# Kernel optimization log

Hardware: AMD Instinct MI355X
Metric: run time of the kernel (lower is better)

## Reference

```python
import jax, jax.numpy as jnp
import numpy as np

D_MODEL = 1024
N_HEAD = 16
HEAD_DIM = D_MODEL // N_HEAD
D_INNER = (int(D_MODEL * 2.0) + 7) // 8 * 8  # 2048
EPS = 1e-6


def setup_inputs() -> dict:
    key = jax.random.key(0)
    ks = jax.random.split(key, 8)
    B, T = 2, 2048
    s = 0.02
    return {
        "x": jax.random.normal(ks[0], (B, T, D_MODEL), dtype=jnp.float32),
        "ln1_w": jnp.ones((D_MODEL,), jnp.float32),
        "ln2_w": jnp.ones((D_MODEL,), jnp.float32),
        "qkv_w": jax.random.normal(ks[1], (3 * D_MODEL, D_MODEL), jnp.float32) * s,
        "o_w": jax.random.normal(ks[2], (D_MODEL, D_MODEL), jnp.float32) * s,
        "gate_w": jax.random.normal(ks[3], (D_INNER, D_MODEL), jnp.float32) * s,
        "up_w": jax.random.normal(ks[4], (D_INNER, D_MODEL), jnp.float32) * s,
        "down_w": jax.random.normal(ks[5], (D_MODEL, D_INNER), jnp.float32) * s,
    }


def _rmsnorm(x, w):
    xf = x.astype(jnp.float32)
    rms = jax.lax.rsqrt(jnp.mean(xf * xf, axis=-1, keepdims=True) + EPS)
    return (xf * rms).astype(x.dtype) * w


def _attention(x, qkv_w, o_w):
    B, T, D = x.shape
    qkv = (x @ qkv_w.T).reshape(B, T, 3, N_HEAD, HEAD_DIM)
    q, k, v = qkv[:, :, 0], qkv[:, :, 1], qkv[:, :, 2]  # [B,T,H,hd]
    scale = 1.0 / np.sqrt(HEAD_DIM)
    att = jnp.einsum("bqhd,bkhd->bhqk", q, k) * scale
    causal = jnp.tril(jnp.ones((T, T), dtype=bool))
    att = jnp.where(causal[None, None], att, -jnp.inf)
    att = jax.nn.softmax(att, axis=-1)
    y = jnp.einsum("bhqk,bkhd->bqhd", att, v).reshape(B, T, D)
    return y @ o_w.T


def _ffn(x, gate_w, up_w, down_w):
    g = jax.nn.silu(x @ gate_w.T)
    u = x @ up_w.T
    return (g * u) @ down_w.T


def reference(x, ln1_w, ln2_w, qkv_w, o_w, gate_w, up_w, down_w):
    x = x + _attention(_rmsnorm(x, ln1_w), qkv_w, o_w)
    x = x + _ffn(_rmsnorm(x, ln2_w), gate_w, up_w, down_w)
    return x
```

## Files before the change

### kernel.cpp

```cpp
#include <hip/hip_runtime.h>
#include <hip/hip_bf16.h>
#include <cstdint>

typedef __hip_bfloat16 bf16;
typedef __attribute__((ext_vector_type(8))) short bf16x8;
typedef __attribute__((ext_vector_type(4))) float f32x4;
typedef __attribute__((ext_vector_type(4))) int i32x4;

#define T_SEQ 2048
#define DMODEL 1024
#define NHEAD 16
#define DHEAD 64
#define MROWS 4096

typedef const __attribute__((address_space(1))) void* gas_ptr;
typedef __attribute__((address_space(3))) void* las_ptr;

static __device__ __forceinline__ f32x4 mfma16(bf16x8 a, bf16x8 b, f32x4 c) {
  return __builtin_amdgcn_mfma_f32_16x16x32_bf16(a, b, c, 0, 0, 0);
}
static __device__ __forceinline__ void gload_lds16(const void* g, void* l) {
  __builtin_amdgcn_global_load_lds((gas_ptr)g, (las_ptr)l, 16, 0, 0);
}
static __device__ __forceinline__ float b2f(unsigned short u) {
  union { unsigned int i; float f; } x; x.i = ((unsigned int)u) << 16; return x.f;
}
static __device__ __forceinline__ unsigned short f2bu(float f) {
  __hip_bfloat16 h = __float2bfloat16(f);
  unsigned short u; __builtin_memcpy(&u, &h, 2); return u;
}
static __device__ __forceinline__ int tpack(float a, float b) {
  const unsigned ua = __builtin_bit_cast(unsigned, a);
  const unsigned ub = __builtin_bit_cast(unsigned, b);
  return (int)((ua >> 16) | (ub & 0xFFFF0000u));
}

__global__ __launch_bounds__(256) void prep_k(const float* __restrict__ a,
                                              const float* __restrict__ b,
                                              const float* __restrict__ c,
                                              const float* __restrict__ d,
                                              const float* __restrict__ e,
                                              bf16* __restrict__ out,
                                              const float* __restrict__ x,
                                              const float* __restrict__ ln1w,
                                              bf16* __restrict__ H) {
  if (blockIdx.x < 10240) {
    const int idx = (blockIdx.x * 256 + threadIdx.x) * 4;
    const float* src;
    int off, dst;
    if (idx < 3145728) {
      src = a; off = idx; dst = idx;
    } else if (idx < 4194304) {
      src = b; off = idx - 3145728; dst = idx;
    } else if (idx < 6291456) {
      src = c; off = idx - 4194304;
      dst = 4194304 + ((off >> 10) << 11) + (off & 1023);
    } else if (idx < 8388608) {
      src = d; off = idx - 6291456;
      dst = 4194304 + ((off >> 10) << 11) + 1024 + (off & 1023);
    } else {
      src = e; off = idx - 8388608; dst = idx;
    }
    const float4 v = *(const float4*)(src + off);
    ushort4 ov;
    ov.x = f2bu(v.x); ov.y = f2bu(v.y); ov.z = f2bu(v.z); ov.w = f2bu(v.w);
    *(ushort4*)((unsigned short*)out + dst) = ov;
  } else {
    const int row = blockIdx.x - 10240;
    const int tid = threadIdx.x;
    const float4 v = ((const float4*)(x + (size_t)row * DMODEL))[tid];
    float ss = v.x * v.x + v.y * v.y + v.z * v.z + v.w * v.w;
#pragma unroll
    for (int off = 32; off; off >>= 1) ss += __shfl_xor(ss, off);
    __shared__ float red[4];
    if ((tid & 63) == 0) red[tid >> 6] = ss;
    __syncthreads();
    const float tot = red[0] + red[1] + red[2] + red[3];
    const float rinv = rsqrtf(tot * (1.f / DMODEL) + 1e-6f);
    const float4 wv = ((const float4*)ln1w)[tid];
    bf16* o = H + (size_t)row * DMODEL + tid * 4;
    o[0] = __float2bfloat16(v.x * rinv * wv.x);
    o[1] = __float2bfloat16(v.y * rinv * wv.y);
    o[2] = __float2bfloat16(v.z * rinv * wv.z);
    o[3] = __float2bfloat16(v.w * rinv * wv.w);
  }
}

__global__ __launch_bounds__(256) void rms_k(const float* __restrict__ x,
                                             const float* __restrict__ w,
                                             bf16* __restrict__ out) {
  const int row = blockIdx.x;
  const int tid = threadIdx.x;
  const float4 v = ((const float4*)(x + (size_t)row * DMODEL))[tid];
  float ss = v.x * v.x + v.y * v.y + v.z * v.z + v.w * v.w;
#pragma unroll
  for (int off = 32; off; off >>= 1) ss += __shfl_xor(ss, off);
  __shared__ float red[4];
  if ((tid & 63) == 0) red[tid >> 6] = ss;
  __syncthreads();
  const float tot = red[0] + red[1] + red[2] + red[3];
  const float rinv = rsqrtf(tot * (1.f / DMODEL) + 1e-6f);
  const float4 wv = ((const float4*)w)[tid];
  bf16* o = out + (size_t)row * DMODEL + tid * 4;
  o[0] = __float2bfloat16(v.x * rinv * wv.x);
  o[1] = __float2bfloat16(v.y * rinv * wv.y);
  o[2] = __float2bfloat16(v.z * rinv * wv.z);
  o[3] = __float2bfloat16(v.w * rinv * wv.w);
}

template <int K, int EPI>
__global__ __launch_bounds__(256) void gemm_bt(const bf16* __restrict__ A,
                                               const bf16* __restrict__ Bw, int N,
                                               void* __restrict__ o0, void* __restrict__ o1,
                                               void* __restrict__ o2,
                                               const float* __restrict__ res) {
  __shared__ bf16 As[128 * 64];
  __shared__ bf16 Bs[128 * 64];
  const int bn0 = blockIdx.x * 128;
  const int bm0 = blockIdx.y * 128;
  const int tid = threadIdx.x;
  const int wave = tid >> 6, lane = tid & 63;
  const int wr = wave >> 1, wc = wave & 1;
  const int fr = lane & 15, u = lane >> 4, r4 = u * 4;
  const int srow = lane >> 3;
  const int sslot = (lane & 7) ^ srow;
  const int fsw = fr & 7;

  const f32x4 fzero = {0.f, 0.f, 0.f, 0.f};
  f32x4 acc[4][4];
#pragma unroll
  for (int i = 0; i < 4; i++)
#pragma unroll
    for (int j = 0; j < 4; j++) acc[i][j] = fzero;

  const bf16* gA = A + (size_t)(bm0 + wave * 32 + srow) * K + sslot * 8;
  const bf16* gB = Bw + (size_t)(bn0 + wave * 32 + srow) * K + sslot * 8;

  for (int k0 = 0; k0 < K; k0 += 64) {
#pragma unroll
    for (int j = 0; j < 4; j++)
      gload_lds16(gA + (size_t)(j * 8) * K + k0, &As[(wave * 32 + j * 8) * 64]);
#pragma unroll
    for (int j = 0; j < 4; j++)
      gload_lds16(gB + (size_t)(j * 8) * K + k0, &Bs[(wave * 32 + j * 8) * 64]);
    __syncthreads();
#pragma unroll
    for (int kh = 0; kh < 2; kh++) {
      const int slot8 = ((kh * 4 + u) ^ fsw) * 8;
      bf16x8 af[4], bfr[4];
#pragma unroll
      for (int mr = 0; mr < 4; mr++)
        af[mr] = *(const bf16x8*)&As[(wr * 64 + mr * 16 + fr) * 64 + slot8];
#pragma unroll
      for (int nr = 0; nr < 4; nr++)
        bfr[nr] = *(const bf16x8*)&Bs[(wc * 64 + nr * 16 + fr) * 64 + slot8];
#pragma unroll
      for (int mr = 0; mr < 4; mr++)
#pragma unroll
        for (int nr = 0; nr < 4; nr++)
          acc[mr][nr] = mfma16(af[mr], bfr[nr], acc[mr][nr]);
    }
    __syncthreads();
  }

#pragma unroll
  for (int mr = 0; mr < 4; mr++) {
#pragma unroll
    for (int nr = 0; nr < 4; nr++) {
      if (EPI == 1) {
        const int col = bn0 + wc * 64 + nr * 16 + fr;
        const int sel = col >> 10;
        const int n = col & 1023;
        const int h = n >> 6, d = n & 63;
        const int row0 = bm0 + wr * 64 + mr * 16 + r4;
        const int b = row0 >> 11, t0 = row0 & 2047;
        if (sel == 2) {
          ushort4 ov;
          ov.x = f2bu(acc[mr][nr][0]);
          ov.y = f2bu(acc[mr][nr][1]);
          ov.z = f2bu(acc[mr][nr][2]);
          ov.w = f2bu(acc[mr][nr][3]);
          *(ushort4*)((unsigned short*)o2 +
                      (((size_t)(b * NHEAD + h)) * DHEAD + d) * T_SEQ + t0) = ov;
        } else {
          bf16* dst = (sel == 0) ? (bf16*)o0 : (bf16*)o1;
#pragma unroll
          for (int r = 0; r < 4; r++)
            dst[(((size_t)(b * NHEAD + h)) * T_SEQ + t0 + r) * DHEAD + d] =
                __float2bfloat16(acc[mr][nr][r]);
        }
      } else {
#pragma unroll
        for (int r = 0; r < 4; r++) {
          const int row = bm0 + wr * 64 + mr * 16 + r4 + r;
          const int col = bn0 + wc * 64 + nr * 16 + fr;
          const float vsum = acc[mr][nr][r];
          if (EPI == 2) {
            ((float*)o0)[(size_t)row * N + col] = res[(size_t)row * N + col] + vsum;
          } else {
            const float other = __shfl_xor(vsum, 1);
            if ((fr & 1) == 0) {
              const float g = vsum, uu = other;
              const float s = g / (1.f + __expf(-g));
              ((bf16*)o0)[(size_t)row * (N >> 1) + (col >> 1)] =
                  __float2bfloat16(s * uu);
            }
          }
        }
      }
    }
  }
}

__global__ __launch_bounds__(256) void attn_k(const bf16* __restrict__ qb,
                                              const bf16* __restrict__ kb,
                                              const bf16* __restrict__ vt,
                                              bf16* __restrict__ y,
                                              unsigned short* __restrict__ pO,
                                              float* __restrict__ pL) {
  const int wave = threadIdx.x >> 6, lane = threadIdx.x & 63;
  const int bid = blockIdx.x;
  int bh, qt, ks0, nb, heavy, hs;
  if (bid < 1024) {
    const int c = bid & 7, r = bid >> 3;
    bh = c * 4 + (r & 3);
    const int idx = r >> 2;
    qt = 31 - (idx >> 1);
    hs = idx & 1;
    heavy = 1;
    nb = qt + 1;
    ks0 = hs * nb;
  } else {
    const int bd = bid - 1024;
    const int c = bd & 7, r = bd >> 3;
    bh = c * 4 + (r & 3);
    qt = 15 - (r >> 2);
    hs = 0;
    heavy = 0;
    nb = 2 * qt + 2;
    ks0 = 0;
  }
  const int b = bh >> 4, h = bh & 15;
  const int fr = lane & 15, g8 = (lane >> 4) * 8, r4 = (lane >> 4) * 4;
  const int u = lane >> 4;
  const int src1 = fr + ((u & 1) << 5);
  const int src2 = src1 + 16;
  const bool hB = u >= 2;

  const bf16* qp = qb + (size_t)bh * T_SEQ * DHEAD;
  const bf16* kp = kb + (size_t)bh * T_SEQ * DHEAD;
  const bf16* vp = vt + (size_t)bh * DHEAD * T_SEQ;

  __shared__ char Ks[2][4096];
  __shared__ char Vs[2][4096];

  const int q0 = qt * 64 + wave * 16;
  const int kend = q0 + 16;
  const int qrow = q0 + fr;

  const bf16x8 qf0 = *(const bf16x8*)(qp + (size_t)(q0 + fr) * DHEAD + g8);
  const bf16x8 qf1 = *(const bf16x8*)(qp + (size_t)(q0 + fr) * DHEAD + 32 + g8);

  const int krow_l = lane >> 3;
  const int kslot_l = (lane & 7) ^ krow_l;
  const int vrow_l = lane >> 2;
  const int vslot_l = (lane & 3) ^ ((lane >> 3) & 3);

  const int kswz = (fr & 7) << 4;
  const int koffA = fr * 128 + ((u * 16) ^ kswz);
  const int koffB = fr * 128 + (((4 + u) * 16) ^ kswz);
  const int vswz = ((fr >> 1) & 3) << 4;

  const f32x4 fzero = {0.f, 0.f, 0.f, 0.f};
  f32x4 acc[4];
  float lpart = 0.f;
#pragma unroll
  for (int nf = 0; nf < 4; nf++) acc[nf] = fzero;

  gload_lds16(kp + (size_t)(ks0 * 32 + wave * 8 + krow_l) * DHEAD + kslot_l * 8,
              &Ks[0][wave * 1024]);
  gload_lds16(vp + (size_t)(wave * 16 + vrow_l) * T_SEQ + ks0 * 32 + vslot_l * 8,
              &Vs[0][wave * 1024]);
  __syncthreads();

  for (int ts = 0; ts < nb; ++ts) {
    const int kt = (ks0 + ts) * 32;
    const int buf = ts & 1;
    if (ts + 1 < nb) {
      const int kn = kt + 32;
      gload_lds16(kp + (size_t)(kn + wave * 8 + krow_l) * DHEAD + kslot_l * 8,
                  &Ks[buf ^ 1][wave * 1024]);
      gload_lds16(vp + (size_t)(wave * 16 + vrow_l) * T_SEQ + kn + vslot_l * 8,
                  &Vs[buf ^ 1][wave * 1024]);
    }
    if (kt < kend) {
      const char* KB = Ks[buf];
      const char* VB = Vs[buf];
      const bf16x8 kf0a = *(const bf16x8*)(KB + koffA);
      const bf16x8 kf0b = *(const bf16x8*)(KB + koffB);
      const bf16x8 kf1a = *(const bf16x8*)(KB + 2048 + koffA);
      const bf16x8 kf1b = *(const bf16x8*)(KB + 2048 + koffB);
      bf16x8 vf[4];
#pragma unroll
      for (int nf = 0; nf < 4; nf++)
        vf[nf] = *(const bf16x8*)(VB + (nf * 16 + fr) * 64 + ((u * 16) ^ vswz));

      f32x4 s0 = mfma16(kf0a, qf0, fzero);
      s0 = mfma16(kf0b, qf1, s0);
      f32x4 s1 = mfma16(kf1a, qf0, fzero);
      s1 = mfma16(kf1b, qf1, s1);

      float x0[4], x1[4];
      if (kt + 31 < q0) {
#pragma unroll
        for (int r = 0; r < 4; r++) {
          x0[r] = __expf(s0[r] * 0.125f);
          x1[r] = __expf(s1[r] * 0.125f);
          lpart += x0[r] + x1[r];
        }
      } else {
#pragma unroll
        for (int r = 0; r < 4; r++) {
          const int k0 = kt + r4 + r;
          const int k1 = k0 + 16;
          x0[r] = (k0 <= qrow) ? __expf(s0[r] * 0.125f) : 0.f;
          x1[r] = (k1 <= qrow) ? __expf(s1[r] * 0.125f) : 0.f;
          lpart += x0[r] + x1[r];
        }
      }

      const int A01 = tpack(x0[0], x0[1]);
      const int A23 = tpack(x0[2], x0[3]);
      const int B01 = tpack(x1[0], x1[1]);
      const int B23 = tpack(x1[2], x1[3]);

      const int t0a = __shfl(A01, src1), t0b = __shfl(B01, src1);
      const int t1a = __shfl(A23, src1), t1b = __shfl(B23, src1);
      const int t2a = __shfl(A01, src2), t2b = __shfl(B01, src2);
      const int t3a = __shfl(A23, src2), t3b = __shfl(B23, src2);
      i32x4 pw;
      pw[0] = hB ? t0b : t0a;
      pw[1] = hB ? t1b : t1a;
      pw[2] = hB ? t2b : t2a;
      pw[3] = hB ? t3b : t3a;
      const bf16x8 pb = __builtin_bit_cast(bf16x8, pw);

#pragma unroll
      for (int nf = 0; nf < 4; nf++) acc[nf] = mfma16(vf[nf], pb, acc[nf]);
    }
    __syncthreads();
  }

  lpart += __shfl_xor(lpart, 16);
  lpart += __shfl_xor(lpart, 32);

  if (!heavy) {
    const float inv = 1.f / lpart;
    const int t = q0 + fr;
    unsigned short* yb =
        (unsigned short*)(y + (((size_t)(b * T_SEQ + t)) * NHEAD + h) * DHEAD);
#pragma unroll
    for (int nf = 0; nf < 4; nf++) {
      ushort4 ov;
      ov.x = f2bu(acc[nf][0] * inv);
      ov.y = f2bu(acc[nf][1] * inv);
      ov.z = f2bu(acc[nf][2] * inv);
      ov.w = f2bu(acc[nf][3] * inv);
      *(ushort4*)(yb + nf * 16 + r4) = ov;
    }
  } else {
    const int tl = q0 - 1024 + fr;
    unsigned short* po = pO + ((size_t)(hs * 32 + bh) * 1024 + tl) * DHEAD;
#pragma unroll
    for (int nf = 0; nf < 4; nf++) {
      ushort4 ov;
      ov.x = f2bu(acc[nf][0]);
      ov.y = f2bu(acc[nf][1]);
      ov.z = f2bu(acc[nf][2]);
      ov.w = f2bu(acc[nf][3]);
      *(ushort4*)(po + nf * 16 + r4) = ov;
    }
    if (lane < 16) pL[(size_t)(hs * 32 + bh) * 1024 + (q0 - 1024) + lane] = lpart;
  }
}

__global__ __launch_bounds__(256) void comb_k(const unsigned short* __restrict__ pO,
                                              const float* __restrict__ pL,
                                              bf16* __restrict__ y) {
  const int idx = blockIdx.x * 256 + threadIdx.x;
  const int row = idx >> 4;
  const int d0 = (idx & 15) * 4;
  const int bh = row >> 10, tl = row & 1023;
  const int b = bh >> 4, h = bh & 15;
  const int t = 1024 + tl;
  const float inv = 1.f / (pL[row] + pL[32768 + row]);
  const ushort4 a = *(const ushort4*)(pO + (size_t)row * DHEAD + d0);
  const ushort4 c = *(const ushort4*)(pO + (size_t)(32768 + row) * DHEAD + d0);
  ushort4 ov;
  ov.x = f2bu((b2f(a.x) + b2f(c.x)) * inv);
  ov.y = f2bu((b2f(a.y) + b2f(c.y)) * inv);
  ov.z = f2bu((b2f(a.z) + b2f(c.z)) * inv);
  ov.w = f2bu((b2f(a.w) + b2f(c.w)) * inv);
  *(ushort4*)((unsigned short*)y + (((size_t)(b * T_SEQ + t)) * NHEAD + h) * DHEAD + d0) = ov;
}

extern "C" void kernel_launch(void* const* d_in, const int* in_sizes, int n_in,
                              void* d_out, int out_size, void* d_ws, size_t ws_size,
                              hipStream_t stream) {
  const float* x     = (const float*)d_in[0];
  const float* ln1w  = (const float*)d_in[1];
  const float* ln2w  = (const float*)d_in[2];
  const float* qkvw  = (const float*)d_in[3];
  const float* ow    = (const float*)d_in[4];
  const float* gatew = (const float*)d_in[5];
  const float* upw   = (const float*)d_in[6];
  const float* downw = (const float*)d_in[7];

  uint8_t* ws = (uint8_t*)d_ws;
  bf16* WQKV = (bf16*)(ws + 0);
  bf16* WO   = (bf16*)(ws + 6291456);
  bf16* WGU  = (bf16*)(ws + 8388608);
  bf16* WD   = (bf16*)(ws + 16777216);
  bf16* H    = (bf16*)(ws + 20971520);
  bf16* Q    = (bf16*)(ws + 29360128);
  bf16* Kb   = (bf16*)(ws + 37748736);
  bf16* VT   = (bf16*)(ws + 46137344);
  bf16* Y    = (bf16*)(ws + 54525952);
  float* X2  = (float*)(ws + 62914560);
  bf16* G = (bf16*)(ws + 29360128);
  unsigned short* pO = (unsigned short*)(ws + 62914560);
  float* pL = (float*)(ws + 20971520);

  prep_k<<<14336, 256, 0, stream>>>(qkvw, ow, gatew, upw, downw, (bf16*)ws,
                                    x, ln1w, H);

  gemm_bt<1024, 1><<<dim3(24, 32), 256, 0, stream>>>(H, WQKV, 3072, Q, Kb, VT, nullptr);
  attn_k<<<1536, 256, 0, stream>>>(Q, Kb, VT, Y, pO, pL);
  comb_k<<<2048, 256, 0, stream>>>(pO, pL, Y);
  gemm_bt<1024, 2><<<dim3(8, 32), 256, 0, stream>>>(Y, WO, 1024, X2, nullptr, nullptr, x);

  rms_k<<<MROWS, 256, 0, stream>>>(X2, ln2w, H);
  gemm_bt<1024, 4><<<dim3(32, 32), 256, 0, stream>>>(H, WGU, 4096, G, nullptr, nullptr, nullptr);
  gemm_bt<2048, 2><<<dim3(8, 32), 256, 0, stream>>>(G, WD, 1024, (float*)d_out, nullptr, nullptr, X2);
}
```

Baseline: 222.3 us.

## Use 64-key attention tiles and fold softmax scale into Q projection

The attention kernel now stages 64 keys per double-buffered LDS step instead of 32 and processes two 32-key halves per step. This halves the number of barriers and loop iterations, and the split ranges for heavy blocks are recomputed to match. The softmax scale times log2(e) is folded into Q in the QKV epilogue so the kernel can call exp2f directly, removing a multiply per score. LDS use per block doubles, which may reduce occupancy. Rounding Q to bf16 after scaling slightly changes numerics.

```diff
diff --git a/kernel.cpp b/kernel.cpp
--- a/kernel.cpp
+++ b/kernel.cpp
@@ -12,6 +12,7 @@
 #define NHEAD 16
 #define DHEAD 64
 #define MROWS 4096
+#define QSCALE 0.18033688011112042f
 
 typedef const __attribute__((address_space(1))) void* gas_ptr;
 typedef __attribute__((address_space(3))) void* las_ptr;
@@ -184,10 +185,11 @@
                       (((size_t)(b * NHEAD + h)) * DHEAD + d) * T_SEQ + t0) = ov;
         } else {
           bf16* dst = (sel == 0) ? (bf16*)o0 : (bf16*)o1;
+          const float sc = (sel == 0) ? QSCALE : 1.f;
 #pragma unroll
           for (int r = 0; r < 4; r++)
             dst[(((size_t)(b * NHEAD + h)) * T_SEQ + t0 + r) * DHEAD + d] =
-                __float2bfloat16(acc[mr][nr][r]);
+                __float2bfloat16(acc[mr][nr][r] * sc);
         }
       } else {
 #pragma unroll
@@ -228,8 +230,10 @@
     qt = 31 - (idx >> 1);
     hs = idx & 1;
     heavy = 1;
-    nb = qt + 1;
-    ks0 = hs * nb;
+    const int nt = qt + 1;
+    const int h1 = (nt + 1) >> 1;
+    ks0 = hs ? h1 : 0;
+    nb = hs ? (nt - h1) : h1;
   } else {
     const int bd = bid - 1024;
     const int c = bd & 7, r = bd >> 3;
@@ -237,7 +241,7 @@
     qt = 15 - (r >> 2);
     hs = 0;
     heavy = 0;
-    nb = 2 * qt + 2;
+    nb = qt + 1;
     ks0 = 0;
   }
   const int b = bh >> 4, h = bh & 15;
@@ -251,8 +255,8 @@
   const bf16* kp = kb + (size_t)bh * T_SEQ * DHEAD;
   const bf16* vp = vt + (size_t)bh * DHEAD * T_SEQ;
 
-  __shared__ char Ks[2][4096];
-  __shared__ char Vs[2][4096];
+  __shared__ char Ks[2][8192];
+  __shared__ char Vs[2][8192];
 
   const int q0 = qt * 64 + wave * 16;
   const int kend = q0 + 16;
@@ -261,15 +265,12 @@
   const bf16x8 qf0 = *(const bf16x8*)(qp + (size_t)(q0 + fr) * DHEAD + g8);
   const bf16x8 qf1 = *(const bf16x8*)(qp + (size_t)(q0 + fr) * DHEAD + 32 + g8);
 
-  const int krow_l = lane >> 3;
-  const int kslot_l = (lane & 7) ^ krow_l;
-  const int vrow_l = lane >> 2;
-  const int vslot_l = (lane & 3) ^ ((lane >> 3) & 3);
+  const int r0 = wave * 16 + (lane >> 3);
+  const int sl8 = (lane & 7) ^ (lane >> 3);
 
   const int kswz = (fr & 7) << 4;
   const int koffA = fr * 128 + ((u * 16) ^ kswz);
   const int koffB = fr * 128 + (((4 + u) * 16) ^ kswz);
-  const int vswz = ((fr >> 1) & 3) << 4;
 
   const f32x4 fzero = {0.f, 0.f, 0.f, 0.f};
   f32x4 acc[4];
@@ -277,76 +278,88 @@
 #pragma unroll
   for (int nf = 0; nf < 4; nf++) acc[nf] = fzero;
 
-  gload_lds16(kp + (size_t)(ks0 * 32 + wave * 8 + krow_l) * DHEAD + kslot_l * 8,
-              &Ks[0][wave * 1024]);
-  gload_lds16(vp + (size_t)(wave * 16 + vrow_l) * T_SEQ + ks0 * 32 + vslot_l * 8,
-              &Vs[0][wave * 1024]);
+  {
+    const int kt = ks0 * 64;
+    gload_lds16(kp + (size_t)(kt + r0) * DHEAD + sl8 * 8, &Ks[0][wave * 2048]);
+    gload_lds16(kp + (size_t)(kt + r0 + 8) * DHEAD + sl8 * 8, &Ks[0][wave * 2048 + 1024]);
+    gload_lds16(vp + (size_t)r0 * T_SEQ + kt + sl8 * 8, &Vs[0][wave * 2048]);
+    gload_lds16(vp + (size_t)(r0 + 8) * T_SEQ + kt + sl8 * 8, &Vs[0][wave * 2048 + 1024]);
+  }
   __syncthreads();
 
   for (int ts = 0; ts < nb; ++ts) {
-    const int kt = (ks0 + ts) * 32;
+    const int kt = (ks0 + ts) * 64;
     const int buf = ts & 1;
     if (ts + 1 < nb) {
-      const int kn = kt + 32;
-      gload_lds16(kp + (size_t)(kn + wave * 8 + krow_l) * DHEAD + kslot_l * 8,
-                  &Ks[buf ^ 1][wave * 1024]);
-      gload_lds16(vp + (size_t)(wave * 16 + vrow_l) * T_SEQ + kn + vslot_l * 8,
-                  &Vs[buf ^ 1][wave * 1024]);
+      const int kn = kt + 64;
+      gload_lds16(kp + (size_t)(kn + r0) * DHEAD + sl8 * 8, &Ks[buf ^ 1][wave * 2048]);
+      gload_lds16(kp + (size_t)(kn + r0 + 8) * DHEAD + sl8 * 8,
+                  &Ks[buf ^ 1][wave * 2048 + 1024]);
+      gload_lds16(vp + (size_t)r0 * T_SEQ + kn + sl8 * 8, &Vs[buf ^ 1][wave * 2048]);
+      gload_lds16(vp + (size_t)(r0 + 8) * T_SEQ + kn + sl8 * 8,
+                  &Vs[buf ^ 1][wave * 2048 + 1024]);
     }
     if (kt < kend) {
       const char* KB = Ks[buf];
       const char* VB = Vs[buf];
-      const bf16x8 kf0a = *(const bf16x8*)(KB + koffA);
-      const bf16x8 kf0b = *(const bf16x8*)(KB + koffB);
-      const bf16x8 kf1a = *(const bf16x8*)(KB + 2048 + koffA);
-      const bf16x8 kf1b = *(const bf16x8*)(KB + 2048 + koffB);
-      bf16x8 vf[4];
-#pragma unroll
-      for (int nf = 0; nf < 4; nf++)
-        vf[nf] = *(const bf16x8*)(VB + (nf * 16 + fr) * 64 + ((u * 16) ^ vswz));
-
-      f32x4 s0 = mfma16(kf0a, qf0, fzero);
-      s0 = mfma16(kf0b, qf1, s0);
-      f32x4 s1 = mfma16(kf1a, qf0, fzero);
-      s1 = mfma16(kf1b, qf1, s1);
-
-      float x0[4], x1[4];
-      if (kt + 31 < q0) {
-#pragma unroll
-        for (int r = 0; r < 4; r++) {
-          x0[r] = __expf(s0[r] * 0.125f);
-          x1[r] = __expf(s1[r] * 0.125f);
-          lpart += x0[r] + x1[r];
-        }
-      } else {
-#pragma unroll
-        for (int r = 0; r < 4; r++) {
-          const int k0 = kt + r4 + r;
-          const int k1 = k0 + 16;
-          x0[r] = (k0 <= qrow) ? __expf(s0[r] * 0.125f) : 0.f;
-          x1[r] = (k1 <= qrow) ? __expf(s1[r] * 0.125f) : 0.f;
-          lpart += x0[r] + x1[r];
+#pragma unroll
+      for (int kh2 = 0; kh2 < 2; kh2++) {
+        const int khalf = kt + kh2 * 32;
+        if (khalf < kend) {
+          const int kb2 = kh2 * 4096;
+          const bf16x8 kf0a = *(const bf16x8*)(KB + kb2 + koffA);
+          const bf16x8 kf0b = *(const bf16x8*)(KB + kb2 + koffB);
+          const bf16x8 kf1a = *(const bf16x8*)(KB + kb2 + 2048 + koffA);
+          const bf16x8 kf1b = *(const bf16x8*)(KB + kb2 + 2048 + koffB);
+
+          f32x4 s0 = mfma16(kf0a, qf0, fzero);
+          s0 = mfma16(kf0b, qf1, s0);
+          f32x4 s1 = mfma16(kf1a, qf0, fzero);
+          s1 = mfma16(kf1b, qf1, s1);
+
+          float x0[4], x1[4];
+          if (khalf + 31 < q0) {
+#pragma unroll
+            for (int r = 0; r < 4; r++) {
+              x0[r] = exp2f(s0[r]);
+              x1[r] = exp2f(s1[r]);
+              lpart += x0[r] + x1[r];
+            }
+          } else {
+#pragma unroll
+            for (int r = 0; r < 4; r++) {
+              const int k0 = khalf + r4 + r;
+              const int k1 = k0 + 16;
+              x0[r] = (k0 <= qrow) ? exp2f(s0[r]) : 0.f;
+              x1[r] = (k1 <= qrow) ? exp2f(s1[r]) : 0.f;
+              lpart += x0[r] + x1[r];
+            }
+          }
+
+          const int A01 = tpack(x0[0], x0[1]);
+          const int A23 = tpack(x0[2], x0[3]);
+          const int B01 = tpack(x1[0], x1[1]);
+          const int B23 = tpack(x1[2], x1[3]);
+
+          const int t0a = __shfl(A01, src1), t0b = __shfl(B01, src1);
+          const int t1a = __shfl(A23, src1), t1b = __shfl(B23, src1);
+          const int t2a = __shfl(A01, src2), t2b = __shfl(B01, src2);
+          const int t3a = __shfl(A23, src2), t3b = __shfl(B23, src2);
+          i32x4 pw;
+          pw[0] = hB ? t0b : t0a;
+          pw[1] = hB ? t1b : t1a;
+          pw[2] = hB ? t2b : t2a;
+          pw[3] = hB ? t3b : t3a;
+          const bf16x8 pb = __builtin_bit_cast(bf16x8, pw);
+
+          const int vls = ((kh2 * 4 + u) ^ (fr & 7)) << 4;
+#pragma unroll
+          for (int nf = 0; nf < 4; nf++) {
+            const bf16x8 vf = *(const bf16x8*)(VB + (nf * 16 + fr) * 128 + vls);
+            acc[nf] = mfma16(vf, pb, acc[nf]);
+          }
         }
       }
-
-      const int A01 = tpack(x0[0], x0[1]);
-      const int A23 = tpack(x0[2], x0[3]);
-      const int B01 = tpack(x1[0], x1[1]);
-      const int B23 = tpack(x1[2], x1[3]);
-
-      const int t0a = __shfl(A01, src1), t0b = __shfl(B01, src1);
-      const int t1a = __shfl(A23, src1), t1b = __shfl(B23, src1);
-      const int t2a = __shfl(A01, src2), t2b = __shfl(B01, src2);
-      const int t3a = __shfl(A23, src2), t3b = __shfl(B23, src2);
-      i32x4 pw;
-      pw[0] = hB ? t0b : t0a;
-      pw[1] = hB ? t1b : t1a;
-      pw[2] = hB ? t2b : t2a;
-      pw[3] = hB ? t3b : t3a;
-      const bf16x8 pb = __builtin_bit_cast(bf16x8, pw);
-
-#pragma unroll
-      for (int nf = 0; nf < 4; nf++) acc[nf] = mfma16(vf[nf], pb, acc[nf]);
     }
     __syncthreads();
   }
```

Result: slower. 232.8 us (+4.7%).
